# Kernel tuning notes

Hardware: AMD Instinct MI355X
Metric: run time of the kernel (lower is better)

The kernel has to match this reference:

```python
import jax, jax.numpy as jnp
import numpy as np

N_NODES = 100000
N_EDGES = 1600000
F_IN, HIDDEN, N_CLS = 128, 128, 40


def _gcn_layer(h, W, b, src, dst, norm, n):
    # h: [n, d_in] -> linear transform then edge-normalized scatter-add
    h = h @ W                                   # [n, d_out]
    msg = h[src] * norm[:, None]                # gather over edges [E', d_out]
    out = jax.ops.segment_sum(msg, dst, num_segments=n)
    return out + b


def setup_inputs() -> dict:
    key = jax.random.key(0)
    k1, k2, k3, k4 = jax.random.split(key, 4)
    x = jax.random.normal(k1, (N_NODES, F_IN), dtype=jnp.float32)
    edge_index = jax.random.randint(k2, (2, N_EDGES), 0, N_NODES, dtype=jnp.int32)
    # glorot-style init
    W1 = jax.random.normal(k3, (F_IN, HIDDEN), dtype=jnp.float32) * (1.0 / np.sqrt(F_IN))
    W2 = jax.random.normal(k4, (HIDDEN, N_CLS), dtype=jnp.float32) * (1.0 / np.sqrt(HIDDEN))
    b1 = jnp.zeros((HIDDEN,), dtype=jnp.float32)
    b2 = jnp.zeros((N_CLS,), dtype=jnp.float32)
    return {"x": x, "edge_index": edge_index, "W1": W1, "b1": b1,
            "W2": W2, "b2": b2, "dropout": 0}


def reference(x, edge_index, W1, b1, W2, b2, dropout):
    n = x.shape[0]
    src, dst = edge_index[0], edge_index[1]
    # add self loops (PyG GCNConv default)
    loop = jnp.arange(n, dtype=src.dtype)
    src = jnp.concatenate([src, loop])
    dst = jnp.concatenate([dst, loop])
    # symmetric normalization D^{-1/2} (A+I) D^{-1/2}
    deg = jax.ops.segment_sum(jnp.ones(src.shape, dtype=x.dtype), dst, num_segments=n)
    dinv = jnp.where(deg > 0, jax.lax.rsqrt(deg), 0.0)
    norm = dinv[src] * dinv[dst]                # [E + n]
    h = jax.nn.relu(_gcn_layer(x, W1, b1, src, dst, norm, n))
    # F.dropout with training=False is identity (eval mode)
    return _gcn_layer(h, W2, b2, src, dst, norm, n)
```

## Files before the change

kernel.cpp:

```cpp
#include <hip/hip_runtime.h>
#include <stdint.h>


#define NF 128
#define NC 40
#define PSHIFT 7
#define PNODES 128
#define GH 256

typedef __attribute__((ext_vector_type(8))) short short8;
typedef __attribute__((ext_vector_type(4))) float float4m;

__device__ __forceinline__ float bflo2f(unsigned int u) {
  union { unsigned int i; float f; } v; v.i = u << 16; return v.f;
}
__device__ __forceinline__ float bfhi2f(unsigned int u) {
  union { unsigned int i; float f; } v; v.i = u & 0xffff0000u; return v.f;
}
__device__ __forceinline__ unsigned short f2bf(float f) {
  union { float f; unsigned int i; } v; v.f = f;
  unsigned int x = v.i;
  return (unsigned short)((x + 0x7fffu + ((x >> 16) & 1u)) >> 16);
}

__device__ __forceinline__ unsigned int rowld64(const unsigned int* __restrict__ B,
                                                int idx, int lane) {
  unsigned int off = ((unsigned)idx << 6) | (unsigned)lane;
  __builtin_assume(off < (1u << 25));
  return B[off];
}
__device__ __forceinline__ unsigned int rowld32(const unsigned int* __restrict__ B,
                                                int idx, int ci) {
  unsigned int off = ((unsigned)idx << 5) | (unsigned)ci;
  __builtin_assume(off < (1u << 23));
  return B[off];
}
__device__ __forceinline__ int4 bidx4(const int4* __restrict__ B, int off) {
  __builtin_assume(off >= 0 && off < (1 << 22));
  return B[off];
}

__global__ __launch_bounds__(256) void hist_pack_k(
    const int* __restrict__ ei, int* __restrict__ histT, int E, int CPB, int NPART,
    const float* __restrict__ W1, const float* __restrict__ W2,
    unsigned short* __restrict__ Bpack, unsigned short* __restrict__ W2pack,
    unsigned int* __restrict__ Hsu, unsigned int* __restrict__ H2u, int n) {
  int tid = threadIdx.x, bid = blockIdx.x;
  if (bid >= GH) {
    int g = (bid - GH) * 256 + tid;
    const float* W; unsigned short* dst; int cols, frag;
    if (g < 2048)      { W = W1; dst = Bpack;  cols = 128; frag = g; }
    else if (g < 2816) { W = W2; dst = W2pack; cols = 40;  frag = g - 2048; }
    else if (g < 2880) { Hsu[(size_t)n * 64 + (g - 2816)] = 0u; return; }
    else if (g < 2912) { H2u[(size_t)n * 32 + (g - 2880)] = 0u; return; }
    else return;
    int ct = frag >> 8, ks = (frag >> 6) & 3, lane = frag & 63;
    int quad = lane >> 4, l15 = lane & 15;
    int col = ct * 16 + l15, krow = ks * 32 + quad * 8;
    ushort4 lo = {0,0,0,0}, hi = {0,0,0,0};
    if (col < cols) {
      lo.x = f2bf(W[(krow + 0) * cols + col]);
      lo.y = f2bf(W[(krow + 1) * cols + col]);
      lo.z = f2bf(W[(krow + 2) * cols + col]);
      lo.w = f2bf(W[(krow + 3) * cols + col]);
      hi.x = f2bf(W[(krow + 4) * cols + col]);
      hi.y = f2bf(W[(krow + 5) * cols + col]);
      hi.z = f2bf(W[(krow + 6) * cols + col]);
      hi.w = f2bf(W[(krow + 7) * cols + col]);
    }
    *(ushort4*)&dst[(size_t)frag * 8 + 0] = lo;
    *(ushort4*)&dst[(size_t)frag * 8 + 4] = hi;
    return;
  }
  __shared__ int h[1024];
  for (int i = tid; i < NPART; i += 256) h[i] = 0;
  __syncthreads();
  int e0 = bid * CPB, e1 = min(e0 + CPB, E);
  for (int e = e0 + tid; e < e1; e += 256)
    atomicAdd(&h[ei[E + e] >> PSHIFT], 1);
  __syncthreads();
  for (int i = tid; i < NPART; i += 256) histT[(size_t)i * GH + bid] = h[i];
}

__global__ __launch_bounds__(256) void scanA_k(int* __restrict__ histT,
                                               int* __restrict__ partTotal) {
  __shared__ int sm[GH];
  int tid = threadIdx.x, p = blockIdx.x;
  int v = histT[(size_t)p * GH + tid];
  sm[tid] = v; __syncthreads();
  for (int off = 1; off < GH; off <<= 1) {
    int t = (tid >= off) ? sm[tid - off] : 0;
    __syncthreads();
    sm[tid] += t;
    __syncthreads();
  }
  histT[(size_t)p * GH + tid] = sm[tid] - v;
  if (tid == GH - 1) partTotal[p] = sm[GH - 1];
}

__global__ __launch_bounds__(1024) void scanB_k(const int* __restrict__ partTotal,
                                                int* __restrict__ base, int NPART) {
  __shared__ int sm[1024];
  int tid = threadIdx.x;
  int v = (tid < NPART) ? partTotal[tid] : 0;
  sm[tid] = v; __syncthreads();
  for (int off = 1; off < 1024; off <<= 1) {
    int t = (tid >= off) ? sm[tid - off] : 0;
    __syncthreads();
    sm[tid] += t;
    __syncthreads();
  }
  if (tid < NPART) base[tid] = sm[tid] - v;
}

__global__ __launch_bounds__(256) void scatter_k(const int* __restrict__ ei,
                                                 const int* __restrict__ histT,
                                                 const int* __restrict__ base,
                                                 unsigned int* __restrict__ epart,
                                                 int E, int CPB, int NPART) {
  __shared__ int off[1024];
  int tid = threadIdx.x, bid = blockIdx.x;
  for (int i = tid; i < NPART; i += 256)
    off[i] = base[i] + histT[(size_t)i * GH + bid];
  __syncthreads();
  int e0 = bid * CPB, e1 = min(e0 + CPB, E);
  for (int e = e0 + tid; e < e1; e += 256) {
    int s = ei[e], d = ei[E + e];
    int pos = atomicAdd(&off[d >> PSHIFT], 1);
    epart[pos] = ((unsigned int)(d & (PNODES - 1)) << 25) | (unsigned int)s;
  }
}

__global__ __launch_bounds__(256) void degpart_k(const unsigned int* __restrict__ epart,
                                                 const int* __restrict__ base,
                                                 const int* __restrict__ partTotal,
                                                 int* __restrict__ deg,
                                                 float* __restrict__ dinv, int n) {
  __shared__ int lcnt[PNODES];
  int tid = threadIdx.x, p = blockIdx.x;
  if (tid < PNODES) lcnt[tid] = 0;
  __syncthreads();
  int st = base[p], m = partTotal[p];
  for (int e = tid; e < m; e += 256)
    atomicAdd(&lcnt[epart[(size_t)st + e] >> 25], 1);
  __syncthreads();
  int node = (p << PSHIFT) + tid;
  if (tid < PNODES && node < n) {
    int c = lcnt[tid];
    deg[node] = c;
    dinv[node] = rsqrtf((float)c + 1.0f);
  }
}

__global__ __launch_bounds__(256, 4) void build_gemm_k(
    const float* __restrict__ x, const unsigned short* __restrict__ Bpack,
    unsigned short* __restrict__ Hs, const unsigned int* __restrict__ epart,
    const int* __restrict__ base, const int* __restrict__ partTotal,
    const float* __restrict__ dinv,
    int* __restrict__ bucket, int n, int NPART, int G1) {
  __shared__ alignas(16) char smem[33792];
  int tid = threadIdx.x, bid = blockIdx.x;

  if (bid % 3 == 2) {
    int pidx = bid / 3;
    if (pidx >= NPART) return;
    int* lcnt = (int*)smem;
    int* lbuck = lcnt + PNODES;
    if (tid < PNODES) lcnt[tid] = 0;
    __syncthreads();
    int st = base[pidx], m = partTotal[pidx];
    for (int e = tid; e < m; e += 256) {
      unsigned int u = epart[(size_t)st + e];
      int ln = (int)(u >> 25), s = (int)(u & 0x1ffffffu);
      int pos = atomicAdd(&lcnt[ln], 1);
      if (pos < 64) lbuck[ln * 64 + pos] = s;
    }
    __syncthreads();
    int node0 = pidx << PSHIFT;
    int nn = min(PNODES, n - node0);
    for (int i = tid; i < nn; i += 256) {
      int c = lcnt[i]; if (c > 64) c = 64;
      int c8 = (c + 7) & ~7; if (c8 > 64) c8 = 64;
      for (int p = c; p < c8; p++) lbuck[i * 64 + p] = n;
    }
    __syncthreads();
    int4* bg = (int4*)&bucket[(size_t)node0 * 64];
    const int4* bl = (const int4*)lbuck;
    for (int i = tid; i < nn * 16; i += 256) {
      int nd = i >> 4, q = i & 15;
      int c = lcnt[nd]; if (c > 64) c = 64;
      int c8 = (c + 7) & ~7; if (c8 > 64) c8 = 64;
      if (q * 4 < c8) bg[i] = bl[i];
    }
    return;
  }

  int idx = (bid / 3) * 2 + (bid % 3);
  if (idx >= G1) return;
  unsigned short* As = (unsigned short*)smem;
  unsigned short* Bs = (unsigned short*)(smem + 17408);
  int r0 = idx * 64;

  const float4* x4 = (const float4*)x;
  for (int i = tid; i < 2048; i += 256) {
    int kc = i & 31, r = i >> 5;
    float4 v = make_float4(0.f, 0.f, 0.f, 0.f);
    if (r0 + r < n) {
      float dr = dinv[r0 + r];
      v = x4[(size_t)(r0 + r) * 32 + kc];
      v.x *= dr; v.y *= dr; v.z *= dr; v.w *= dr;
    }
    ushort4 o;
    o.x = f2bf(v.x); o.y = f2bf(v.y); o.z = f2bf(v.z); o.w = f2bf(v.w);
    *(ushort4*)&As[r * 136 + kc * 4] = o;
  }
  const uint4* bp4 = (const uint4*)Bpack;
  uint4* bs4 = (uint4*)Bs;
  for (int i = tid; i < 1024; i += 256) bs4[i] = bp4[i];
  __syncthreads();

  int wv = tid >> 6, lane = tid & 63;
  int quad = lane >> 4, l15 = lane & 15;

  short8 afr[4];
#pragma unroll
  for (int ks = 0; ks < 4; ks++)
    afr[ks] = *(const short8*)&As[(wv * 16 + l15) * 136 + ks * 32 + quad * 8];

  float4m acc[8];
#pragma unroll
  for (int i = 0; i < 8; i++) acc[i] = (float4m){0.f, 0.f, 0.f, 0.f};

#pragma unroll
  for (int ct = 0; ct < 4; ct++) {
#pragma unroll
    for (int ks = 0; ks < 4; ks++) {
      short8 bfr = *(const short8*)&Bs[(((ct * 4 + ks) * 64) + lane) * 8];
      acc[ct] = __builtin_amdgcn_mfma_f32_16x16x32_bf16(afr[ks], bfr, acc[ct], 0, 0, 0);
    }
  }
  __syncthreads();
  for (int i = tid; i < 1024; i += 256) bs4[i] = bp4[1024 + i];
  __syncthreads();
#pragma unroll
  for (int ct = 4; ct < 8; ct++) {
#pragma unroll
    for (int ks = 0; ks < 4; ks++) {
      short8 bfr = *(const short8*)&Bs[((((ct - 4) * 4 + ks) * 64) + lane) * 8];
      acc[ct] = __builtin_amdgcn_mfma_f32_16x16x32_bf16(afr[ks], bfr, acc[ct], 0, 0, 0);
    }
  }

  __syncthreads();
  unsigned short* Cs = (unsigned short*)smem;
  int rloc = wv * 16 + quad * 4;
#pragma unroll
  for (int ct = 0; ct < 8; ct++) {
#pragma unroll
    for (int reg = 0; reg < 4; reg++)
      Cs[(rloc + reg) * 128 + ct * 16 + l15] = f2bf(acc[ct][reg]);
  }
  __syncthreads();
  uint4* HsV = (uint4*)Hs;
  const uint4* CsV = (const uint4*)Cs;
  for (int i = tid; i < 1024; i += 256) {
    int r = i >> 4;
    if (r0 + r < n) HsV[(size_t)(r0 + r) * 16 + (i & 15)] = CsV[i];
  }
}

__global__ __launch_bounds__(256, 8) void agg1f_k(const unsigned int* __restrict__ Hs2,
                                               const int* __restrict__ deg,
                                               const int* __restrict__ bucket,
                                               const float* __restrict__ dinv,
                                               const float2* __restrict__ b1v,
                                               const unsigned short* __restrict__ W2pack,
                                               unsigned short* __restrict__ H2s, int n) {
  __shared__ unsigned short As[16 * 136];
  __shared__ unsigned short W2s[768 * 8];
  int tid = threadIdx.x, wv = tid >> 6, lane = tid & 63;
  int node0 = blockIdx.x * 16;

  {
    const uint4* p = (const uint4*)W2pack;
    uint4* q = (uint4*)W2s;
    for (int i = tid; i < 768; i += 256) q[i] = p[i];
  }

  float2 bv = b1v[lane];
  const int4* bucket4 = (const int4*)bucket;

  for (int s = 0; s < 4; s++) {
    int mrow = wv * 4 + s;
    int node = node0 + mrow;
    float r0 = 0.f, r1 = 0.f;
    if (node < n) {
      float d = dinv[node];
      unsigned int v = rowld64(Hs2, node, lane);
      float a0 = bflo2f(v), a1 = bfhi2f(v);
      int m = deg[node]; if (m > 64) m = 64;
      int m8 = (m + 7) & ~7;
      int bq0 = node * 16;
      int p = 0;
      for (; p + 15 < m8; p += 16) {
        int4 qa = bidx4(bucket4, bq0 + (p >> 2) + 0);
        int4 qb = bidx4(bucket4, bq0 + (p >> 2) + 1);
        int4 qc = bidx4(bucket4, bq0 + (p >> 2) + 2);
        int4 qd = bidx4(bucket4, bq0 + (p >> 2) + 3);
        unsigned int u0  = rowld64(Hs2, qa.x, lane);
        unsigned int u1  = rowld64(Hs2, qa.y, lane);
        unsigned int u2  = rowld64(Hs2, qa.z, lane);
        unsigned int u3  = rowld64(Hs2, qa.w, lane);
        unsigned int u4  = rowld64(Hs2, qb.x, lane);
        unsigned int u5  = rowld64(Hs2, qb.y, lane);
        unsigned int u6  = rowld64(Hs2, qb.z, lane);
        unsigned int u7  = rowld64(Hs2, qb.w, lane);
        unsigned int u8  = rowld64(Hs2, qc.x, lane);
        unsigned int u9  = rowld64(Hs2, qc.y, lane);
        unsigned int u10 = rowld64(Hs2, qc.z, lane);
        unsigned int u11 = rowld64(Hs2, qc.w, lane);
        unsigned int u12 = rowld64(Hs2, qd.x, lane);
        unsigned int u13 = rowld64(Hs2, qd.y, lane);
        unsigned int u14 = rowld64(Hs2, qd.z, lane);
        unsigned int u15 = rowld64(Hs2, qd.w, lane);
        a0 += bflo2f(u0)  + bflo2f(u1)  + bflo2f(u2)  + bflo2f(u3)
            + bflo2f(u4)  + bflo2f(u5)  + bflo2f(u6)  + bflo2f(u7)
            + bflo2f(u8)  + bflo2f(u9)  + bflo2f(u10) + bflo2f(u11)
            + bflo2f(u12) + bflo2f(u13) + bflo2f(u14) + bflo2f(u15);
        a1 += bfhi2f(u0)  + bfhi2f(u1)  + bfhi2f(u2)  + bfhi2f(u3)
            + bfhi2f(u4)  + bfhi2f(u5)  + bfhi2f(u6)  + bfhi2f(u7)
            + bfhi2f(u8)  + bfhi2f(u9)  + bfhi2f(u10) + bfhi2f(u11)
            + bfhi2f(u12) + bfhi2f(u13) + bfhi2f(u14) + bfhi2f(u15);
      }
      if (p < m8) {
        int4 qa = bidx4(bucket4, bq0 + (p >> 2) + 0);
        int4 qb = bidx4(bucket4, bq0 + (p >> 2) + 1);
        unsigned int u0 = rowld64(Hs2, qa.x, lane);
        unsigned int u1 = rowld64(Hs2, qa.y, lane);
        unsigned int u2 = rowld64(Hs2, qa.z, lane);
        unsigned int u3 = rowld64(Hs2, qa.w, lane);
        unsigned int u4 = rowld64(Hs2, qb.x, lane);
        unsigned int u5 = rowld64(Hs2, qb.y, lane);
        unsigned int u6 = rowld64(Hs2, qb.z, lane);
        unsigned int u7 = rowld64(Hs2, qb.w, lane);
        a0 += bflo2f(u0) + bflo2f(u1) + bflo2f(u2) + bflo2f(u3)
            + bflo2f(u4) + bflo2f(u5) + bflo2f(u6) + bflo2f(u7);
        a1 += bfhi2f(u0) + bfhi2f(u1) + bfhi2f(u2) + bfhi2f(u3)
            + bfhi2f(u4) + bfhi2f(u5) + bfhi2f(u6) + bfhi2f(u7);
      }
      r0 = fmaxf(0.0f, bv.x + d * a0);
      r1 = fmaxf(0.0f, bv.y + d * a1);
    }
    unsigned int pk = (unsigned int)f2bf(r0) | ((unsigned int)f2bf(r1) << 16);
    *(unsigned int*)&As[mrow * 136 + lane * 2] = pk;
  }
  __syncthreads();

  if (wv < 3) {
    int quad = lane >> 4, l15 = lane & 15;
    float4m acc = (float4m){0.f, 0.f, 0.f, 0.f};
#pragma unroll
    for (int ks = 0; ks < 4; ks++) {
      short8 afr = *(const short8*)&As[l15 * 136 + ks * 32 + quad * 8];
      short8 bfr = *(const short8*)&W2s[(((wv * 4 + ks) * 64) + lane) * 8];
      acc = __builtin_amdgcn_mfma_f32_16x16x32_bf16(afr, bfr, acc, 0, 0, 0);
    }
    int c = wv * 16 + l15;
    if (c < NC) {
#pragma unroll
      for (int reg = 0; reg < 4; reg++) {
        int node = node0 + quad * 4 + reg;
        if (node < n) {
          float dd = dinv[node];
          H2s[(size_t)node * 64 + c] = f2bf(acc[reg] * dd);
        }
      }
    }
  }
}

__global__ __launch_bounds__(256) void agg2_k(const unsigned int* __restrict__ H2u,
                                              const int* __restrict__ deg,
                                              const int* __restrict__ bucket,
                                              const float* __restrict__ dinv,
                                              const float* __restrict__ b2,
                                              float* __restrict__ outp, int n) {
  int w = (blockIdx.x * 256 + threadIdx.x) >> 6;
  int lane = threadIdx.x & 63;
  int sub = lane / 20, ci = lane - sub * 20;
  int node = w * 3 + sub;
  if (sub >= 3 || node >= n) return;

  float d = dinv[node];
  unsigned int u = rowld32(H2u, node, ci);
  float a0 = bflo2f(u), a1 = bfhi2f(u);

  int m = deg[node]; if (m > 64) m = 64;
  int m8 = (m + 7) & ~7;
  const int4* bucket4 = (const int4*)bucket;
  int bq0 = node * 16;
  int p = 0;
  for (; p + 15 < m8; p += 16) {
    int4 qa = bidx4(bucket4, bq0 + (p >> 2) + 0);
    int4 qb = bidx4(bucket4, bq0 + (p >> 2) + 1);
    int4 qc = bidx4(bucket4, bq0 + (p >> 2) + 2);
    int4 qd = bidx4(bucket4, bq0 + (p >> 2) + 3);
    unsigned int u0  = rowld32(H2u, qa.x, ci);
    unsigned int u1  = rowld32(H2u, qa.y, ci);
    unsigned int u2  = rowld32(H2u, qa.z, ci);
    unsigned int u3  = rowld32(H2u, qa.w, ci);
    unsigned int u4  = rowld32(H2u, qb.x, ci);
    unsigned int u5  = rowld32(H2u, qb.y, ci);
    unsigned int u6  = rowld32(H2u, qb.z, ci);
    unsigned int u7  = rowld32(H2u, qb.w, ci);
    unsigned int u8  = rowld32(H2u, qc.x, ci);
    unsigned int u9  = rowld32(H2u, qc.y, ci);
    unsigned int u10 = rowld32(H2u, qc.z, ci);
    unsigned int u11 = rowld32(H2u, qc.w, ci);
    unsigned int u12 = rowld32(H2u, qd.x, ci);
    unsigned int u13 = rowld32(H2u, qd.y, ci);
    unsigned int u14 = rowld32(H2u, qd.z, ci);
    unsigned int u15 = rowld32(H2u, qd.w, ci);
    a0 += bflo2f(u0) +bflo2f(u1) +bflo2f(u2) +bflo2f(u3)
        + bflo2f(u4) +bflo2f(u5) +bflo2f(u6) +bflo2f(u7)
        + bflo2f(u8) +bflo2f(u9) +bflo2f(u10)+bflo2f(u11)
        + bflo2f(u12)+bflo2f(u13)+bflo2f(u14)+bflo2f(u15);
    a1 += bfhi2f(u0) +bfhi2f(u1) +bfhi2f(u2) +bfhi2f(u3)
        + bfhi2f(u4) +bfhi2f(u5) +bfhi2f(u6) +bfhi2f(u7)
        + bfhi2f(u8) +bfhi2f(u9) +bfhi2f(u10)+bfhi2f(u11)
        + bfhi2f(u12)+bfhi2f(u13)+bfhi2f(u14)+bfhi2f(u15);
  }
  if (p < m8) {
    int4 qa = bidx4(bucket4, bq0 + (p >> 2) + 0);
    int4 qb = bidx4(bucket4, bq0 + (p >> 2) + 1);
    unsigned int u0 = rowld32(H2u, qa.x, ci);
    unsigned int u1 = rowld32(H2u, qa.y, ci);
    unsigned int u2 = rowld32(H2u, qa.z, ci);
    unsigned int u3 = rowld32(H2u, qa.w, ci);
    unsigned int u4 = rowld32(H2u, qb.x, ci);
    unsigned int u5 = rowld32(H2u, qb.y, ci);
    unsigned int u6 = rowld32(H2u, qb.z, ci);
    unsigned int u7 = rowld32(H2u, qb.w, ci);
    a0 += bflo2f(u0)+bflo2f(u1)+bflo2f(u2)+bflo2f(u3)
        + bflo2f(u4)+bflo2f(u5)+bflo2f(u6)+bflo2f(u7);
    a1 += bfhi2f(u0)+bfhi2f(u1)+bfhi2f(u2)+bfhi2f(u3)
        + bfhi2f(u4)+bfhi2f(u5)+bfhi2f(u6)+bfhi2f(u7);
  }

  float2 o;
  o.x = b2[2 * ci]     + d * a0;
  o.y = b2[2 * ci + 1] + d * a1;
  *(float2*)&outp[(size_t)node * 40 + 2 * ci] = o;
}

extern "C" void kernel_launch(void* const* d_in, const int* in_sizes, int n_in,
                              void* d_out, int out_size, void* d_ws, size_t ws_size,
                              hipStream_t stream) {
  const float* x  = (const float*)d_in[0];
  const int*   ei = (const int*)d_in[1];
  const float* W1 = (const float*)d_in[2];
  const float* b1 = (const float*)d_in[3];
  const float* W2 = (const float*)d_in[4];
  const float* b2 = (const float*)d_in[5];

  int N = in_sizes[0] / NF;
  int E = in_sizes[1] / 2;
  int NPART = (N + PNODES - 1) >> PSHIFT;
  int CPB = (E + GH - 1) / GH;
  int G1 = (N + 63) / 64;

  char* ws = (char*)d_ws;
  size_t off = 0;
  auto carve = [&](size_t bytes) {
    void* p = ws + off;
    off += (bytes + 255) & ~(size_t)255;
    return p;
  };
  int*            deg       = (int*)carve((size_t)N * 4);
  float*          dinv      = (float*)carve((size_t)N * 4);
  int*            bucket    = (int*)carve((size_t)N * 64 * 4);
  unsigned short* Hs        = (unsigned short*)carve((size_t)(N + 1) * NF * 2);
  int*            histT     = (int*)carve((size_t)NPART * GH * 4);
  int*            partTotal = (int*)carve((size_t)NPART * 4);
  int*            base      = (int*)carve((size_t)NPART * 4);
  unsigned int*   epart     = (unsigned int*)carve((size_t)E * 4);
  unsigned short* Bpack     = (unsigned short*)carve(2048 * 8 * 2);
  unsigned short* W2pack    = (unsigned short*)carve(768 * 8 * 2);
  unsigned short* H2s       = (unsigned short*)carve((size_t)(N + 1) * 64 * 2);

  hist_pack_k<<<GH + 12, 256, 0, stream>>>(ei, histT, E, CPB, NPART,
                                           W1, W2, Bpack, W2pack,
                                           (unsigned int*)Hs, (unsigned int*)H2s, N);
  scanA_k<<<NPART, 256, 0, stream>>>(histT, partTotal);
  scanB_k<<<1, 1024, 0, stream>>>(partTotal, base, NPART);
  scatter_k<<<GH, 256, 0, stream>>>(ei, histT, base, epart, E, CPB, NPART);
  degpart_k<<<NPART, 256, 0, stream>>>(epart, base, partTotal, deg, dinv, N);
  build_gemm_k<<<3 * NPART, 256, 0, stream>>>(x, Bpack, Hs, epart, base, partTotal,
                                              dinv, bucket, N, NPART, G1);
  agg1f_k<<<(N + 15) / 16, 256, 0, stream>>>((const unsigned int*)Hs, deg, bucket,
                                             dinv, (const float2*)b1, W2pack, H2s, N);
  int NW = (N + 2) / 3;
  agg2_k<<<((size_t)NW * 64 + 255) / 256, 256, 0, stream>>>((const unsigned int*)H2s,
                                                            deg, bucket, dinv, b2,
                                                            (float*)d_out, N);
}
```

Before: 253.8 us.

## Fuse degree computation into bucket build, split GEMM into its own kernel

Merges the degree/dinv kernel with the per-partition bucket build, so epart is read once and the degree and bucket lists come from the same shared-memory pass. The GEMM becomes a separate kernel launched afterwards, where it previously shared a combined launch with the bucket build. This removes one pass over the partitioned edge list but loses the overlap of bucket build and GEMM inside a single launch, and the GEMM now waits for the whole build to finish.

```diff
diff --git a/kernel.cpp b/kernel.cpp
--- a/kernel.cpp
+++ b/kernel.cpp
@@ -131,75 +131,56 @@
   }
 }
 
-__global__ __launch_bounds__(256) void degpart_k(const unsigned int* __restrict__ epart,
-                                                 const int* __restrict__ base,
-                                                 const int* __restrict__ partTotal,
-                                                 int* __restrict__ deg,
-                                                 float* __restrict__ dinv, int n) {
+__global__ __launch_bounds__(256) void build_k(const unsigned int* __restrict__ epart,
+                                               const int* __restrict__ base,
+                                               const int* __restrict__ partTotal,
+                                               int* __restrict__ deg,
+                                               float* __restrict__ dinv,
+                                               int* __restrict__ bucket, int n) {
   __shared__ int lcnt[PNODES];
-  int tid = threadIdx.x, p = blockIdx.x;
+  __shared__ int lbuck[PNODES * 64];
+  int tid = threadIdx.x, pidx = blockIdx.x;
   if (tid < PNODES) lcnt[tid] = 0;
   __syncthreads();
-  int st = base[p], m = partTotal[p];
-  for (int e = tid; e < m; e += 256)
-    atomicAdd(&lcnt[epart[(size_t)st + e] >> 25], 1);
-  __syncthreads();
-  int node = (p << PSHIFT) + tid;
-  if (tid < PNODES && node < n) {
+  int st = base[pidx], m = partTotal[pidx];
+  for (int e = tid; e < m; e += 256) {
+    unsigned int u = epart[(size_t)st + e];
+    int ln = (int)(u >> 25), s = (int)(u & 0x1ffffffu);
+    int pos = atomicAdd(&lcnt[ln], 1);
+    if (pos < 64) lbuck[ln * 64 + pos] = s;
+  }
+  __syncthreads();
+  int node0 = pidx << PSHIFT;
+  int nn = min(PNODES, n - node0);
+  if (tid < nn) {
     int c = lcnt[tid];
-    deg[node] = c;
-    dinv[node] = rsqrtf((float)c + 1.0f);
-  }
-}
-
-__global__ __launch_bounds__(256, 4) void build_gemm_k(
+    deg[node0 + tid] = c;
+    dinv[node0 + tid] = rsqrtf((float)c + 1.0f);
+  }
+  for (int i = tid; i < nn; i += 256) {
+    int c = lcnt[i]; if (c > 64) c = 64;
+    int c8 = (c + 7) & ~7; if (c8 > 64) c8 = 64;
+    for (int p = c; p < c8; p++) lbuck[i * 64 + p] = n;
+  }
+  __syncthreads();
+  int4* bg = (int4*)&bucket[(size_t)node0 * 64];
+  const int4* bl = (const int4*)lbuck;
+  for (int i = tid; i < nn * 16; i += 256) {
+    int nd = i >> 4, q = i & 15;
+    int c = lcnt[nd]; if (c > 64) c = 64;
+    int c8 = (c + 7) & ~7; if (c8 > 64) c8 = 64;
+    if (q * 4 < c8) bg[i] = bl[i];
+  }
+}
+
+__global__ __launch_bounds__(256, 4) void gemm1_k(
     const float* __restrict__ x, const unsigned short* __restrict__ Bpack,
-    unsigned short* __restrict__ Hs, const unsigned int* __restrict__ epart,
-    const int* __restrict__ base, const int* __restrict__ partTotal,
-    const float* __restrict__ dinv,
-    int* __restrict__ bucket, int n, int NPART, int G1) {
+    unsigned short* __restrict__ Hs, const float* __restrict__ dinv, int n) {
   __shared__ alignas(16) char smem[33792];
-  int tid = threadIdx.x, bid = blockIdx.x;
-
-  if (bid % 3 == 2) {
-    int pidx = bid / 3;
-    if (pidx >= NPART) return;
-    int* lcnt = (int*)smem;
-    int* lbuck = lcnt + PNODES;
-    if (tid < PNODES) lcnt[tid] = 0;
-    __syncthreads();
-    int st = base[pidx], m = partTotal[pidx];
-    for (int e = tid; e < m; e += 256) {
-      unsigned int u = epart[(size_t)st + e];
-      int ln = (int)(u >> 25), s = (int)(u & 0x1ffffffu);
-      int pos = atomicAdd(&lcnt[ln], 1);
-      if (pos < 64) lbuck[ln * 64 + pos] = s;
-    }
-    __syncthreads();
-    int node0 = pidx << PSHIFT;
-    int nn = min(PNODES, n - node0);
-    for (int i = tid; i < nn; i += 256) {
-      int c = lcnt[i]; if (c > 64) c = 64;
-      int c8 = (c + 7) & ~7; if (c8 > 64) c8 = 64;
-      for (int p = c; p < c8; p++) lbuck[i * 64 + p] = n;
-    }
-    __syncthreads();
-    int4* bg = (int4*)&bucket[(size_t)node0 * 64];
-    const int4* bl = (const int4*)lbuck;
-    for (int i = tid; i < nn * 16; i += 256) {
-      int nd = i >> 4, q = i & 15;
-      int c = lcnt[nd]; if (c > 64) c = 64;
-      int c8 = (c + 7) & ~7; if (c8 > 64) c8 = 64;
-      if (q * 4 < c8) bg[i] = bl[i];
-    }
-    return;
-  }
-
-  int idx = (bid / 3) * 2 + (bid % 3);
-  if (idx >= G1) return;
+  int tid = threadIdx.x;
   unsigned short* As = (unsigned short*)smem;
   unsigned short* Bs = (unsigned short*)(smem + 17408);
-  int r0 = idx * 64;
+  int r0 = blockIdx.x * 64;
 
   const float4* x4 = (const float4*)x;
   for (int i = tid; i < 2048; i += 256) {
@@ -494,9 +475,8 @@
   scanA_k<<<NPART, 256, 0, stream>>>(histT, partTotal);
   scanB_k<<<1, 1024, 0, stream>>>(partTotal, base, NPART);
   scatter_k<<<GH, 256, 0, stream>>>(ei, histT, base, epart, E, CPB, NPART);
-  degpart_k<<<NPART, 256, 0, stream>>>(epart, base, partTotal, deg, dinv, N);
-  build_gemm_k<<<3 * NPART, 256, 0, stream>>>(x, Bpack, Hs, epart, base, partTotal,
-                                              dinv, bucket, N, NPART, G1);
+  build_k<<<NPART, 256, 0, stream>>>(epart, base, partTotal, deg, dinv, bucket, N);
+  gemm1_k<<<G1, 256, 0, stream>>>(x, Bpack, Hs, dinv, N);
   agg1f_k<<<(N + 15) / 16, 256, 0, stream>>>((const unsigned int*)Hs, deg, bucket,
                                              dinv, (const float2*)b1, W2pack, H2s, N);
   int NW = (N + 2) / 3;
```

After: 245.7 us. 1.03x faster.
